# Optimization experiments

Hardware: AMD Instinct MI355X
Metric: run time of the kernel (lower is better)

Reference implementation:

```python
import jax, jax.numpy as jnp
import numpy as np

# dimensions (match init_kwargs / input_specs)
K = 25        # number of observation events
N_PER = 2048  # observations per event
B = 4096      # batch (sample_idx length)
D = 64        # input_dim
NDIM = 8      # memory_dim
H = D * NDIM  # hidden = 512
STEPS = 2     # euler ODE steps between consecutive obs_times
DT = 0.01
LOG_SQRT_2PI = 0.9189385332046727  # log(sqrt(2*pi))


def _xavier(key, shape):
    lim = np.sqrt(6.0 / (shape[0] + shape[1])).astype(np.float32)
    return jax.random.uniform(key, shape, jnp.float32, -lim, lim)


def setup_inputs() -> dict:
    key = jax.random.key(0)
    ks = jax.random.split(key, 10)
    # unique per-event indices (matches torch scatter-assign semantics)
    rng = np.random.RandomState(0)
    batch_idx = jnp.asarray(
        np.stack([rng.permutation(B)[:N_PER] for _ in range(K)]).reshape(-1),
        jnp.int32)
    return {
        "obs_times": jnp.arange(1, K + 1, dtype=jnp.float32) * (STEPS * DT),
        "event_pt": jnp.arange(K + 1, dtype=jnp.int32) * N_PER,
        "sample_idx": jnp.arange(B, dtype=jnp.int32),
        "X": jax.random.normal(ks[0], (K * N_PER, D), jnp.float32),
        "M": (jax.random.uniform(ks[1], (K * N_PER, D)) < 0.8).astype(jnp.float32),
        "batch_idx": batch_idx,
        # ODEFunc: Linear(H,H) -> Tanh -> Linear(H,H)
        "W_ode1": _xavier(ks[2], (H, H)), "b_ode1": jnp.zeros((H,), jnp.float32),
        "W_ode2": _xavier(ks[3], (H, H)), "b_ode2": jnp.zeros((H,), jnp.float32),
        # GRUCell(D, H)
        "W_ih": _xavier(ks[4], (3 * H, D)), "W_hh": _xavier(ks[5], (3 * H, H)),
        "b_ih": jnp.zeros((3 * H,), jnp.float32), "b_hh": jnp.zeros((3 * H,), jnp.float32),
        # p_model: Linear(H,H) -> ReLU -> (dropout=0) -> Linear(H, 2D)
        "Wp1": _xavier(ks[6], (H, H)), "bp1": jnp.zeros((H,), jnp.float32),
        "Wp2": _xavier(ks[7], (2 * D, H)), "bp2": jnp.zeros((2 * D,), jnp.float32),
    }


def reference(obs_times, event_pt, sample_idx, X, M, batch_idx,
              W_ode1, b_ode1, W_ode2, b_ode2,
              W_ih, W_hh, b_ih, b_hh, Wp1, bp1, Wp2, bp2):
    Xr = X.reshape(K, N_PER, D)
    Mr = M.reshape(K, N_PER, D)
    idx = batch_idx.reshape(K, N_PER)

    def ode_func(h):  # Linear -> Tanh -> Linear
        return jnp.tanh(h @ W_ode1.T + b_ode1) @ W_ode2.T + b_ode2

    def gru(x, h):  # torch GRUCell
        gi = x @ W_ih.T + b_ih
        gh = h @ W_hh.T + b_hh
        i_r, i_z, i_n = jnp.split(gi, 3, axis=1)
        h_r, h_z, h_n = jnp.split(gh, 3, axis=1)
        r = jax.nn.sigmoid(i_r + h_r)
        z = jax.nn.sigmoid(i_z + h_z)
        n = jnp.tanh(i_n + r * h_n)
        return (1.0 - z) * n + z * h

    def event_step(carry, inp):
        h, loss, m_tot = carry
        X_obs, M_obs, i_obs = inp
        # euler odeint over [0, dt], STEPS times to reach obs_time
        for _ in range(STEPS):
            h = h + DT * ode_func(h)
        # likelihood head on all samples, gather observed ones
        p = jax.nn.relu(h @ Wp1.T + bp1) @ Wp2.T + bp2       # [B, 2D]
        p_obs = p[i_obs]                                      # [N_PER, 2D]
        mean, logvar = jnp.split(p_obs, 2, axis=1)
        sigma = jnp.exp(0.5 * logvar)
        error = (X_obs - mean) / sigma
        losses = 0.5 * ((error * error + logvar + 2.0 * LOG_SQRT_2PI) * M_obs)
        # GRU update only on observed indices (scatter)
        h = h.at[i_obs].set(gru(X_obs, h[i_obs]))
        return (h, loss + losses.sum(), m_tot + M_obs.sum()), None

    h0 = jnp.zeros((B, H), jnp.float32)
    (h, loss, m_tot), _ = jax.lax.scan(event_step, (h0, jnp.float32(0.0), jnp.float32(0.0)), (Xr, Mr, idx))
    return (loss / m_tot, jnp.float32(0.0))
```

## Files before the change

kernel.cpp:

```cpp
#include <hip/hip_runtime.h>
#include <cstdint>
#include <cstddef>

#define BATCH 4096
#define DIM 64
#define HID 512
#define NPER 2048
#define KEV 25
#define DT_C 0.01f
#define LOG_SQRT_2PI_C 0.9189385332046727f

typedef __attribute__((ext_vector_type(8))) short short8;
typedef __attribute__((ext_vector_type(4))) float f32x4;

#define MFMA(a, b, c) __builtin_amdgcn_mfma_f32_16x16x32_bf16(a, b, c, 0, 0, 0)
#define BARRIER() __builtin_amdgcn_s_barrier()
#define SCHED0()  __builtin_amdgcn_sched_barrier(0)

__device__ __forceinline__ ushort f2bf(float f) {
    uint32_t u = __float_as_uint(f);
    u += 0x7FFF + ((u >> 16) & 1);
    return (ushort)(u >> 16);
}
__device__ __forceinline__ float sigmoidf_(float x) { return 1.0f / (1.0f + expf(-x)); }

__device__ __forceinline__ void gload_lds16(const ushort* g, ushort* l) {
    __builtin_amdgcn_global_load_lds(
        (const __attribute__((address_space(1))) void*)g,
        (__attribute__((address_space(3))) void*)l, 16, 0, 0);
}
__device__ __forceinline__ void wait_vm(int n) {
    if (n == 8)      asm volatile("s_waitcnt vmcnt(8)" ::: "memory");
    else if (n == 7) asm volatile("s_waitcnt vmcnt(7)" ::: "memory");
    else if (n == 6) asm volatile("s_waitcnt vmcnt(6)" ::: "memory");
    else if (n == 4) asm volatile("s_waitcnt vmcnt(4)" ::: "memory");
    else             asm volatile("s_waitcnt vmcnt(0)" ::: "memory");
}

__device__ __forceinline__ short8 frag64(const ushort* lds, int row, int ks, int lane) {
    int slot = ((ks << 2) + (lane >> 4)) ^ (row & 7);
    return *(const short8*)&lds[row * 64 + slot * 8];
}
__device__ __forceinline__ short8 frag128(const ushort* lds, int row, int ks, int lane) {
    int slot = ((ks << 2) + (lane >> 4)) ^ (row & 7);
    return *(const short8*)&lds[row * 128 + slot * 8];
}

__device__ __forceinline__ void stage128(
    const ushort* g, int row0, int k0, int w, int lane, ushort* lds)
{
    #pragma unroll
    for (int gg = 0; gg < 4; ++gg) {
        int row = row0 + w * 16 + gg * 4 + (lane >> 4);
        int slot = (lane & 15) ^ (row & 7);
        gload_lds16(g + (size_t)row * HID + k0 + slot * 8,
                    &lds[(w * 16 + gg * 4) * 128]);
    }
}

__device__ __forceinline__ void gemm_bk128(
    ushort* A0, ushort* A1, ushort* B0, ushort* B1,
    int w, int lane, int wr, int wc,
    const ushort* Ag, int arow0, const ushort* Bg, int brow0,
    f32x4 acc[2][2])
{
    stage128(Ag, arow0, 0, w, lane, A0);
    stage128(Bg, brow0, 0, w, lane, B0);
    stage128(Ag, arow0, 128, w, lane, A1);
    stage128(Bg, brow0, 128, w, lane, B1);
    for (int t = 0; t < 4; ++t) {
        wait_vm((t < 3) ? 8 : 0);
        BARRIER();
        SCHED0();
        const ushort* Ab = (t & 1) ? A1 : A0;
        const ushort* Bb = (t & 1) ? B1 : B0;
        short8 af[2][4], bf[2][4];
        #pragma unroll
        for (int mi = 0; mi < 2; ++mi) {
            int r = wr * 32 + mi * 16 + (lane & 15);
            #pragma unroll
            for (int ks = 0; ks < 4; ++ks) af[mi][ks] = frag128(Ab, r, ks, lane);
        }
        #pragma unroll
        for (int ni = 0; ni < 2; ++ni) {
            int c = wc * 32 + ni * 16 + (lane & 15);
            #pragma unroll
            for (int ks = 0; ks < 4; ++ks) bf[ni][ks] = frag128(Bb, c, ks, lane);
        }
        #pragma unroll
        for (int ks = 0; ks < 4; ++ks)
            #pragma unroll
            for (int mi = 0; mi < 2; ++mi)
                #pragma unroll
                for (int ni = 0; ni < 2; ++ni)
                    acc[mi][ni] = MFMA(af[mi][ks], bf[ni][ks], acc[mi][ni]);
        SCHED0();
        BARRIER();
        if (t + 2 < 4) {
            stage128(Ag, arow0, (t + 2) * 128, w, lane, (t & 1) ? A1 : A0);
            stage128(Bg, brow0, (t + 2) * 128, w, lane, (t & 1) ? B1 : B0);
        }
    }
}

__global__ __launch_bounds__(256) void fuse1(
    const ushort* __restrict__ hb, const ushort* __restrict__ W1,
    const float* __restrict__ b1, ushort* __restrict__ tbb,
    const ushort* __restrict__ hgb, const ushort* __restrict__ Wp1,
    const float* __restrict__ bp1, ushort* __restrict__ qb, int mode)
{
    __shared__ __align__(16) ushort smem[32768];
    ushort* A0 = smem;         ushort* A1 = smem + 8192;
    ushort* B0 = smem + 16384; ushort* B1 = smem + 24576;
    const int tid = threadIdx.x, lane = tid & 63, w = tid >> 6;
    const int wr = w >> 1, wc = w & 1;
    const int bid = blockIdx.x;

    bool isQ; int b;
    if (mode == 2)      { isQ = true;  b = bid; }
    else if (bid < 512) { isQ = false; b = bid; }
    else                { isQ = true;  b = bid - 512; }
    const ushort* A = isQ ? hgb : hb;
    const ushort* W = isQ ? Wp1 : W1;
    const float* bias = isQ ? bp1 : b1;
    const int r0 = (b >> 3) * 64, c0 = (b & 7) * 64;

    f32x4 acc[2][2] = {};
    gemm_bk128(A0, A1, B0, B1, w, lane, wr, wc, A, r0, W, c0, acc);

    #pragma unroll
    for (int mi = 0; mi < 2; ++mi)
        #pragma unroll
        for (int ni = 0; ni < 2; ++ni) {
            const int c = c0 + wc * 32 + ni * 16 + (lane & 15);
            const float bv = bias[c];
            #pragma unroll
            for (int ii = 0; ii < 4; ++ii) {
                const int r = r0 + wr * 32 + mi * 16 + ((lane >> 4) << 2) + ii;
                const size_t o = (size_t)r * HID + c;
                float v = acc[mi][ni][ii] + bv;
                if (!isQ) tbb[o] = f2bf(tanhf(v));
                else      qb[o]  = f2bf(fmaxf(v, 0.0f));
            }
        }
}

__global__ __launch_bounds__(256) void fuse2(
    const ushort* __restrict__ tbb, const ushort* __restrict__ W2,
    const float* __restrict__ b2, float* __restrict__ h, ushort* __restrict__ hb,
    const int* __restrict__ inv, ushort* __restrict__ hgb,
    const ushort* __restrict__ qb, const ushort* __restrict__ Wp2,
    const float* __restrict__ bp2, const float* __restrict__ Xp,
    const float* __restrict__ Mp, float* __restrict__ sums, int mode)
{
    __shared__ __align__(16) ushort smem[32768];
    const int tid = threadIdx.x, lane = tid & 63, w = tid >> 6;
    const int wr = w >> 1, wc = w & 1;
    const int bid = blockIdx.x;

    bool isP; int b;
    if (mode == 2)      { isP = true;  b = bid; }
    else if (bid < 512) { isP = false; b = bid; }
    else                { isP = true;  b = bid - 512; }

    if (!isP) {
        ushort* A0 = smem;         ushort* A1 = smem + 8192;
        ushort* B0 = smem + 16384; ushort* B1 = smem + 24576;
        const int r0 = (b >> 3) * 64, c0 = (b & 7) * 64;
        f32x4 acc[2][2] = {};
        gemm_bk128(A0, A1, B0, B1, w, lane, wr, wc, tbb, r0, W2, c0, acc);
        #pragma unroll
        for (int mi = 0; mi < 2; ++mi)
            #pragma unroll
            for (int ni = 0; ni < 2; ++ni) {
                const int c = c0 + wc * 32 + ni * 16 + (lane & 15);
                const float bv = b2[c];
                #pragma unroll
                for (int ii = 0; ii < 4; ++ii) {
                    const int r = r0 + wr * 32 + mi * 16 + ((lane >> 4) << 2) + ii;
                    const size_t o = (size_t)r * HID + c;
                    float nh = h[o] + DT_C * (acc[mi][ni][ii] + bv);
                    h[o] = nh;
                    ushort bv16 = f2bf(nh);
                    hb[o] = bv16;
                    if (inv) {
                        int iv = inv[r];
                        if (iv >= 0) hgb[(size_t)iv * HID + c] = bv16;
                    }
                }
            }
        return;
    }

    ushort* A0 = smem;        ushort* A1 = smem + 4096;
    ushort* B0 = smem + 8192; ushort* B1 = smem + 16384;
    const int srow = lane >> 3, sg = ((lane & 7) ^ srow) << 3;
    const int r0t = b * 64;
    const int arow = w * 16 + srow;

    auto stage = [&](int bb, int k0) {
        ushort* A = bb ? A1 : A0; ushort* B = bb ? B1 : B0;
        gload_lds16(qb + (size_t)(r0t + arow) * HID + k0 + sg, &A[(w * 16) * 64]);
        gload_lds16(qb + (size_t)(r0t + arow + 8) * HID + k0 + sg, &A[(w * 16 + 8) * 64]);
        #pragma unroll
        for (int j = 0; j < 4; ++j) {
            int g = w * 4 + j;
            int rw = g * 8 + srow;
            gload_lds16(Wp2 + (size_t)rw * HID + k0 + (((lane & 7) ^ (rw & 7)) << 3),
                        &B[g * 8 * 64]);
        }
    };
    f32x4 acc[2][4] = {};
    stage(0, 0);
    stage(1, 64);
    for (int t = 0; t < 8; ++t) {
        wait_vm((t < 7) ? 6 : 0);
        BARRIER();
        SCHED0();
        const ushort* Ab = (t & 1) ? A1 : A0;
        const ushort* Bb = (t & 1) ? B1 : B0;
        short8 af[2][2], bf[4][2];
        #pragma unroll
        for (int mi = 0; mi < 2; ++mi) {
            int r = wr * 32 + mi * 16 + (lane & 15);
            af[mi][0] = frag64(Ab, r, 0, lane);
            af[mi][1] = frag64(Ab, r, 1, lane);
        }
        #pragma unroll
        for (int ni = 0; ni < 4; ++ni) {
            int c = wc * 64 + ni * 16 + (lane & 15);
            bf[ni][0] = frag64(Bb, c, 0, lane);
            bf[ni][1] = frag64(Bb, c, 1, lane);
        }
        #pragma unroll
        for (int ks = 0; ks < 2; ++ks)
            #pragma unroll
            for (int mi = 0; mi < 2; ++mi)
                #pragma unroll
                for (int ni = 0; ni < 4; ++ni)
                    acc[mi][ni] = MFMA(af[mi][ks], bf[ni][ks], acc[mi][ni]);
        SCHED0();
        BARRIER();
        if (t + 2 < 8) stage(t & 1, (t + 2) * 64);
    }

    float* Plds = (float*)smem;
    #pragma unroll
    for (int mi = 0; mi < 2; ++mi)
        #pragma unroll
        for (int ni = 0; ni < 4; ++ni) {
            int c = wc * 64 + ni * 16 + (lane & 15);
            float bv = bp2[c];
            #pragma unroll
            for (int ii = 0; ii < 4; ++ii) {
                int r = wr * 32 + mi * 16 + ((lane >> 4) << 2) + ii;
                Plds[r * 128 + c] = acc[mi][ni][ii] + bv;
            }
        }
    __syncthreads();

    float local = 0.0f;
    for (int t = tid; t < 64 * 64; t += 256) {
        int r = t >> 6, jj = t & 63;
        float mean = Plds[r * 128 + jj];
        float lv   = Plds[r * 128 + 64 + jj];
        int g = r0t + r;
        float err = (Xp[(size_t)g * 64 + jj] - mean) * expf(-0.5f * lv);
        local += 0.5f * (err * err + lv + 2.0f * LOG_SQRT_2PI_C) * Mp[(size_t)g * 64 + jj];
    }
    #pragma unroll
    for (int o = 32; o > 0; o >>= 1) local += __shfl_down(local, o);
    if (lane == 0) atomicAdd(sums, local);
}

__global__ __launch_bounds__(256) void gru_all(
    const ushort* __restrict__ hgb, const ushort* __restrict__ Xbk,
    const int* __restrict__ idx,
    const ushort* __restrict__ Whh, const ushort* __restrict__ Wih,
    const float* __restrict__ bih, const float* __restrict__ bhh,
    float* __restrict__ h, ushort* __restrict__ hb)
{
    __shared__ __align__(16) ushort smem[28672];
    const int tid = threadIdx.x, lane = tid & 63, w = tid >> 6;
    const int srow = lane >> 3, sg = ((lane & 7) ^ srow) << 3;
    const int bid = blockIdx.x;
    const int r0t = (bid >> 3) * 32, c0 = (bid & 7) * 64;

    auto stage = [&](int b, int p) {
        ushort* A = smem + b * 2048;
        ushort* B = smem + 4096 + b * 12288;
        if (p < 8) {
            gload_lds16(hgb + (size_t)(r0t + w * 8 + srow) * HID + p * 64 + sg,
                        &A[(w * 8) * 64]);
            #pragma unroll
            for (int j = 0; j < 6; ++j) {
                int glid = w * 6 + j;
                int g = glid >> 3, rg = (glid & 7) * 8 + srow;
                gload_lds16(Whh + (size_t)(g * 512 + c0 + rg) * HID + p * 64 + sg,
                            &B[glid * 8 * 64]);
            }
        } else {
            gload_lds16(Xbk + (size_t)(r0t + w * 8 + srow) * DIM + sg, &A[(w * 8) * 64]);
            #pragma unroll
            for (int j = 0; j < 6; ++j) {
                int glid = w * 6 + j;
                int g = glid >> 3, rg = (glid & 7) * 8 + srow;
                gload_lds16(Wih + (size_t)(g * 512 + c0 + rg) * DIM + sg,
                            &B[glid * 8 * 64]);
            }
        }
    };

    f32x4 aR[2] = {}, aZ[2] = {}, aNh[2] = {}, aNx[2] = {};
    stage(0, 0);
    stage(1, 1);
    for (int t = 0; t < 8; ++t) {
        wait_vm((t < 7) ? 7 : 7);
        BARRIER();
        SCHED0();
        const ushort* Ab = smem + (t & 1) * 2048;
        short8 af[2][2];
        #pragma unroll
        for (int mi = 0; mi < 2; ++mi) {
            int r = mi * 16 + (lane & 15);
            af[mi][0] = frag64(Ab, r, 0, lane);
            af[mi][1] = frag64(Ab, r, 1, lane);
        }
        const int c_l = w * 16 + (lane & 15);
        #pragma unroll
        for (int g = 0; g < 3; ++g) {
            const ushort* Bb = smem + 4096 + (t & 1) * 12288 + g * 4096;
            short8 bf0 = frag64(Bb, c_l, 0, lane);
            short8 bf1 = frag64(Bb, c_l, 1, lane);
            #pragma unroll
            for (int mi = 0; mi < 2; ++mi) {
                f32x4& a = (g == 0) ? aR[mi] : (g == 1) ? aZ[mi] : aNh[mi];
                a = MFMA(af[mi][0], bf0, a);
                a = MFMA(af[mi][1], bf1, a);
            }
        }
        SCHED0();
        BARRIER();
        if (t + 2 <= 8) stage(t & 1, t + 2);
    }
    {
        wait_vm(0);
        BARRIER();
        SCHED0();
        const ushort* Ab = smem;
        short8 af[2][2];
        #pragma unroll
        for (int mi = 0; mi < 2; ++mi) {
            int r = mi * 16 + (lane & 15);
            af[mi][0] = frag64(Ab, r, 0, lane);
            af[mi][1] = frag64(Ab, r, 1, lane);
        }
        const int c_l = w * 16 + (lane & 15);
        #pragma unroll
        for (int g = 0; g < 3; ++g) {
            const ushort* Bb = smem + 4096 + g * 4096;
            short8 bf0 = frag64(Bb, c_l, 0, lane);
            short8 bf1 = frag64(Bb, c_l, 1, lane);
            #pragma unroll
            for (int mi = 0; mi < 2; ++mi) {
                f32x4& a = (g == 0) ? aR[mi] : (g == 1) ? aZ[mi] : aNx[mi];
                a = MFMA(af[mi][0], bf0, a);
                a = MFMA(af[mi][1], bf1, a);
            }
        }
    }

    {
        const int c = c0 + w * 16 + (lane & 15);
        const float bR = bih[c] + bhh[c];
        const float bZ = bih[512 + c] + bhh[512 + c];
        const float bNx = bih[1024 + c], bNh = bhh[1024 + c];
        #pragma unroll
        for (int mi = 0; mi < 2; ++mi)
            #pragma unroll
            for (int ii = 0; ii < 4; ++ii) {
                const int iobs = r0t + mi * 16 + ((lane >> 4) << 2) + ii;
                const int gr = idx[iobs];
                float r = sigmoidf_(aR[mi][ii] + bR);
                float z = sigmoidf_(aZ[mi][ii] + bZ);
                float n = tanhf(aNx[mi][ii] + bNx + r * (aNh[mi][ii] + bNh));
                const size_t o = (size_t)gr * HID + c;
                float nh = (1.0f - z) * n + z * h[o];
                h[o] = nh;
                hb[o] = f2bf(nh);
            }
    }
}

__device__ __forceinline__ void block_atomic_sum(float v, float* acc) {
    __shared__ float red[4];
    #pragma unroll
    for (int off = 32; off > 0; off >>= 1) v += __shfl_down(v, off);
    int lane = threadIdx.x & 63, wid = threadIdx.x >> 6;
    if (lane == 0) red[wid] = v;
    __syncthreads();
    if (threadIdx.x == 0) atomicAdd(acc, red[0] + red[1] + red[2] + red[3]);
}

__global__ __launch_bounds__(256) void f2b4_kernel(
    const float* __restrict__ s, ushort* __restrict__ d, int n4)
{
    int t = blockIdx.x * 256 + threadIdx.x;
    if (t >= n4) return;
    float4 v = ((const float4*)s)[t];
    ushort4 o; o.x = f2bf(v.x); o.y = f2bf(v.y); o.z = f2bf(v.z); o.w = f2bf(v.w);
    ((ushort4*)d)[t] = o;
}

__global__ __launch_bounds__(256) void msum_kernel(
    const float* __restrict__ M, int n, float* __restrict__ m_acc)
{
    float v = 0.0f;
    for (int t = blockIdx.x * 256 + threadIdx.x; t < n; t += gridDim.x * 256)
        v += M[t];
    block_atomic_sum(v, m_acc);
}

__global__ __launch_bounds__(256) void inv_scatter(
    const int* __restrict__ bidx, int* __restrict__ inv)
{
    int t = blockIdx.x * 256 + threadIdx.x;
    if (t >= KEV * NPER) return;
    int e = t >> 11, i = t & (NPER - 1);
    inv[(size_t)e * BATCH + bidx[t]] = i;
}

__global__ void finalize_kernel(const float* __restrict__ sums, float* __restrict__ out) {
    if (threadIdx.x == 0) { out[0] = sums[0] / sums[1]; out[1] = 0.0f; }
}

extern "C" void kernel_launch(void* const* d_in, const int* in_sizes, int n_in,
                              void* d_out, int out_size, void* d_ws, size_t ws_size,
                              hipStream_t stream) {
    const float* X      = (const float*)d_in[3];
    const float* M      = (const float*)d_in[4];
    const int* batch_idx= (const int*)  d_in[5];
    const float* W_ode1 = (const float*)d_in[6];
    const float* b_ode1 = (const float*)d_in[7];
    const float* W_ode2 = (const float*)d_in[8];
    const float* b_ode2 = (const float*)d_in[9];
    const float* W_ih   = (const float*)d_in[10];
    const float* W_hh   = (const float*)d_in[11];
    const float* b_ih   = (const float*)d_in[12];
    const float* b_hh   = (const float*)d_in[13];
    const float* Wp1    = (const float*)d_in[14];
    const float* bp1    = (const float*)d_in[15];
    const float* Wp2    = (const float*)d_in[16];
    const float* bp2    = (const float*)d_in[17];
    float* out = (float*)d_out;

    float* ws    = (float*)d_ws;
    float* h     = ws;
    float* sums  = h + (size_t)BATCH * HID;
    int*   inv   = (int*)(sums + 16);
    ushort* hb   = (ushort*)(inv + (size_t)KEV * BATCH);
    ushort* tbb  = hb  + (size_t)BATCH * HID;
    ushort* qb   = tbb + (size_t)BATCH * HID;
    ushort* hgb  = qb  + (size_t)NPER * HID;
    ushort* Xb   = hgb + (size_t)NPER * HID;
    ushort* W1b  = Xb  + (size_t)KEV * NPER * DIM;
    ushort* W2b  = W1b + (size_t)HID * HID;
    ushort* Wp1b = W2b + (size_t)HID * HID;
    ushort* Wp2b = Wp1b + (size_t)HID * HID;
    ushort* Wihb = Wp2b + (size_t)2 * DIM * HID;
    ushort* Whhb = Wihb + (size_t)3 * HID * DIM;

    hipMemsetAsync(h,    0, (size_t)BATCH * HID * sizeof(float), stream);
    hipMemsetAsync(hb,   0, (size_t)BATCH * HID * sizeof(ushort), stream);
    hipMemsetAsync(sums, 0, 2 * sizeof(float), stream);
    hipMemsetAsync(inv,  0xFF, (size_t)KEV * BATCH * sizeof(int), stream);

    dim3 blk(256);
    auto cvt = [&](const float* s, ushort* d, size_t n) {
        f2b4_kernel<<<dim3((unsigned)((n / 4 + 255) / 256)), blk, 0, stream>>>(s, d, (int)(n / 4));
    };
    cvt(W_ode1, W1b,  (size_t)HID * HID);
    cvt(W_ode2, W2b,  (size_t)HID * HID);
    cvt(Wp1,    Wp1b, (size_t)HID * HID);
    cvt(Wp2,    Wp2b, (size_t)2 * DIM * HID);
    cvt(W_ih,   Wihb, (size_t)3 * HID * DIM);
    cvt(W_hh,   Whhb, (size_t)3 * HID * HID);
    cvt(X,      Xb,   (size_t)KEV * NPER * DIM);

    msum_kernel<<<1024, blk, 0, stream>>>(M, KEV * NPER * DIM, sums + 1);
    inv_scatter<<<(KEV * NPER + 255) / 256, blk, 0, stream>>>(batch_idx, inv);

    for (int k = 0; k < KEV; ++k) {
        const ushort* Xbk = Xb + (size_t)k * NPER * DIM;
        const int*   idxk = batch_idx + (size_t)k * NPER;
        int* invk = inv + (size_t)k * BATCH;
        const float* Xp = X + (size_t)(k > 0 ? k - 1 : 0) * NPER * DIM;
        const float* Mp = M + (size_t)(k > 0 ? k - 1 : 0) * NPER * DIM;
        const int m1 = (k > 0) ? 1 : 0;

        fuse1<<<dim3(m1 ? 768 : 512), blk, 0, stream>>>(
            hb, W1b, b_ode1, tbb, hgb, Wp1b, bp1, qb, m1);
        fuse2<<<dim3(m1 ? 544 : 512), blk, 0, stream>>>(
            tbb, W2b, b_ode2, h, hb, nullptr, hgb,
            qb, Wp2b, bp2, Xp, Mp, sums, m1);
        fuse1<<<dim3(512), blk, 0, stream>>>(
            hb, W1b, b_ode1, tbb, hgb, Wp1b, bp1, qb, 0);
        fuse2<<<dim3(512), blk, 0, stream>>>(
            tbb, W2b, b_ode2, h, hb, invk, hgb,
            qb, Wp2b, bp2, Xp, Mp, sums, 0);
        gru_all<<<dim3(512), blk, 0, stream>>>(
            hgb, Xbk, idxk, Whhb, Wihb, b_ih, b_hh, h, hb);
    }

    {
        const float* Xp = X + (size_t)(KEV - 1) * NPER * DIM;
        const float* Mp = M + (size_t)(KEV - 1) * NPER * DIM;
        fuse1<<<dim3(256), blk, 0, stream>>>(
            hb, W1b, b_ode1, tbb, hgb, Wp1b, bp1, qb, 2);
        fuse2<<<dim3(32), blk, 0, stream>>>(
            tbb, W2b, b_ode2, h, hb, nullptr, hgb,
            qb, Wp2b, bp2, Xp, Mp, sums, 2);
    }

    finalize_kernel<<<1, 64, 0, stream>>>(sums, out);
}
```

Baseline: 1.943 ms.

## Restructure GRU kernel: load weights directly to registers, halve row tile

The GRU kernel no longer stages the Whh/Wih weight tiles through LDS. Each lane now reads its B fragments straight from global memory into registers and double-buffers them in registers. Only the small activation tile goes through LDS. The row tile shrinks from 32 to 16, doubling the grid to 1024 blocks, which cuts LDS footprint and raises parallelism but reduces weight reuse per block. Global weight loads are uncoalesced per-lane 16-byte reads and rely on caching, and traffic to the weights doubles.

```diff
diff --git a/kernel.cpp b/kernel.cpp
--- a/kernel.cpp
+++ b/kernel.cpp
@@ -31,7 +31,6 @@
 }
 __device__ __forceinline__ void wait_vm(int n) {
     if (n == 8)      asm volatile("s_waitcnt vmcnt(8)" ::: "memory");
-    else if (n == 7) asm volatile("s_waitcnt vmcnt(7)" ::: "memory");
     else if (n == 6) asm volatile("s_waitcnt vmcnt(6)" ::: "memory");
     else if (n == 4) asm volatile("s_waitcnt vmcnt(4)" ::: "memory");
     else             asm volatile("s_waitcnt vmcnt(0)" ::: "memory");
@@ -44,6 +43,10 @@
 __device__ __forceinline__ short8 frag128(const ushort* lds, int row, int ks, int lane) {
     int slot = ((ks << 2) + (lane >> 4)) ^ (row & 7);
     return *(const short8*)&lds[row * 128 + slot * 8];
+}
+__device__ __forceinline__ short8 bglob(const ushort* B, int col, int ldb, int k0, int ks, int lane) {
+    int slot = (ks << 2) + (lane >> 4);
+    return *(const short8*)&B[(size_t)col * ldb + k0 + slot * 8];
 }
 
 __device__ __forceinline__ void stage128(
@@ -280,115 +283,75 @@
     const float* __restrict__ bih, const float* __restrict__ bhh,
     float* __restrict__ h, ushort* __restrict__ hb)
 {
-    __shared__ __align__(16) ushort smem[28672];
+    __shared__ __align__(16) ushort Asm[2][16 * 64];
     const int tid = threadIdx.x, lane = tid & 63, w = tid >> 6;
     const int srow = lane >> 3, sg = ((lane & 7) ^ srow) << 3;
     const int bid = blockIdx.x;
-    const int r0t = (bid >> 3) * 32, c0 = (bid & 7) * 64;
-
-    auto stage = [&](int b, int p) {
-        ushort* A = smem + b * 2048;
-        ushort* B = smem + 4096 + b * 12288;
-        if (p < 8) {
-            gload_lds16(hgb + (size_t)(r0t + w * 8 + srow) * HID + p * 64 + sg,
-                        &A[(w * 8) * 64]);
-            #pragma unroll
-            for (int j = 0; j < 6; ++j) {
-                int glid = w * 6 + j;
-                int g = glid >> 3, rg = (glid & 7) * 8 + srow;
-                gload_lds16(Whh + (size_t)(g * 512 + c0 + rg) * HID + p * 64 + sg,
-                            &B[glid * 8 * 64]);
+    const int r0t = (bid >> 3) * 16, c0 = (bid & 7) * 64;
+    const int cB = c0 + w * 16 + (lane & 15);
+
+    auto stageA = [&](int b, int p) {
+        if (w < 2) {
+            const ushort* src = (p < 8)
+                ? hgb + (size_t)(r0t + w * 8 + srow) * HID + p * 64 + sg
+                : Xbk + (size_t)(r0t + w * 8 + srow) * DIM + sg;
+            gload_lds16(src, &Asm[b][(w * 8) * 64]);
+        }
+    };
+    short8 bcur[3][2], bnxt[3][2];
+    auto loadB = [&](short8 d[3][2], int p) {
+        #pragma unroll
+        for (int g = 0; g < 3; ++g)
+            #pragma unroll
+            for (int ks = 0; ks < 2; ++ks)
+                d[g][ks] = (p < 8)
+                    ? bglob(Whh, g * 512 + cB, HID, p * 64, ks, lane)
+                    : bglob(Wih, g * 512 + cB, DIM, 0, ks, lane);
+    };
+
+    f32x4 aR = {}, aZ = {}, aNh = {}, aNx = {};
+    stageA(0, 0);
+    loadB(bcur, 0);
+    stageA(1, 1);
+    __syncthreads();
+
+    #pragma unroll
+    for (int t = 0; t < 9; ++t) {
+        if (t < 8) loadB(bnxt, t + 1);
+        const ushort* Ab = &Asm[t & 1][0];
+        short8 af0 = frag64(Ab, lane & 15, 0, lane);
+        short8 af1 = frag64(Ab, lane & 15, 1, lane);
+        aR = MFMA(af0, bcur[0][0], aR); aR = MFMA(af1, bcur[0][1], aR);
+        aZ = MFMA(af0, bcur[1][0], aZ); aZ = MFMA(af1, bcur[1][1], aZ);
+        if (t < 8) { aNh = MFMA(af0, bcur[2][0], aNh); aNh = MFMA(af1, bcur[2][1], aNh); }
+        else       { aNx = MFMA(af0, bcur[2][0], aNx); aNx = MFMA(af1, bcur[2][1], aNx); }
+        if (t < 8) {
+            #pragma unroll
+            for (int g = 0; g < 3; ++g) {
+                bcur[g][0] = bnxt[g][0];
+                bcur[g][1] = bnxt[g][1];
             }
-        } else {
-            gload_lds16(Xbk + (size_t)(r0t + w * 8 + srow) * DIM + sg, &A[(w * 8) * 64]);
-            #pragma unroll
-            for (int j = 0; j < 6; ++j) {
-                int glid = w * 6 + j;
-                int g = glid >> 3, rg = (glid & 7) * 8 + srow;
-                gload_lds16(Wih + (size_t)(g * 512 + c0 + rg) * DIM + sg,
-                            &B[glid * 8 * 64]);
-            }
-        }
-    };
-
-    f32x4 aR[2] = {}, aZ[2] = {}, aNh[2] = {}, aNx[2] = {};
-    stage(0, 0);
-    stage(1, 1);
-    for (int t = 0; t < 8; ++t) {
-        wait_vm((t < 7) ? 7 : 7);
-        BARRIER();
-        SCHED0();
-        const ushort* Ab = smem + (t & 1) * 2048;
-        short8 af[2][2];
-        #pragma unroll
-        for (int mi = 0; mi < 2; ++mi) {
-            int r = mi * 16 + (lane & 15);
-            af[mi][0] = frag64(Ab, r, 0, lane);
-            af[mi][1] = frag64(Ab, r, 1, lane);
-        }
-        const int c_l = w * 16 + (lane & 15);
-        #pragma unroll
-        for (int g = 0; g < 3; ++g) {
-            const ushort* Bb = smem + 4096 + (t & 1) * 12288 + g * 4096;
-            short8 bf0 = frag64(Bb, c_l, 0, lane);
-            short8 bf1 = frag64(Bb, c_l, 1, lane);
-            #pragma unroll
-            for (int mi = 0; mi < 2; ++mi) {
-                f32x4& a = (g == 0) ? aR[mi] : (g == 1) ? aZ[mi] : aNh[mi];
-                a = MFMA(af[mi][0], bf0, a);
-                a = MFMA(af[mi][1], bf1, a);
-            }
-        }
-        SCHED0();
-        BARRIER();
-        if (t + 2 <= 8) stage(t & 1, t + 2);
-    }
+            __syncthreads();
+            stageA(t & 1, t + 2);
+        }
+    }
+
     {
-        wait_vm(0);
-        BARRIER();
-        SCHED0();
-        const ushort* Ab = smem;
-        short8 af[2][2];
-        #pragma unroll
-        for (int mi = 0; mi < 2; ++mi) {
-            int r = mi * 16 + (lane & 15);
-            af[mi][0] = frag64(Ab, r, 0, lane);
-            af[mi][1] = frag64(Ab, r, 1, lane);
-        }
-        const int c_l = w * 16 + (lane & 15);
-        #pragma unroll
-        for (int g = 0; g < 3; ++g) {
-            const ushort* Bb = smem + 4096 + g * 4096;
-            short8 bf0 = frag64(Bb, c_l, 0, lane);
-            short8 bf1 = frag64(Bb, c_l, 1, lane);
-            #pragma unroll
-            for (int mi = 0; mi < 2; ++mi) {
-                f32x4& a = (g == 0) ? aR[mi] : (g == 1) ? aZ[mi] : aNx[mi];
-                a = MFMA(af[mi][0], bf0, a);
-                a = MFMA(af[mi][1], bf1, a);
-            }
-        }
-    }
-
-    {
-        const int c = c0 + w * 16 + (lane & 15);
-        const float bR = bih[c] + bhh[c];
-        const float bZ = bih[512 + c] + bhh[512 + c];
-        const float bNx = bih[1024 + c], bNh = bhh[1024 + c];
-        #pragma unroll
-        for (int mi = 0; mi < 2; ++mi)
-            #pragma unroll
-            for (int ii = 0; ii < 4; ++ii) {
-                const int iobs = r0t + mi * 16 + ((lane >> 4) << 2) + ii;
-                const int gr = idx[iobs];
-                float r = sigmoidf_(aR[mi][ii] + bR);
-                float z = sigmoidf_(aZ[mi][ii] + bZ);
-                float n = tanhf(aNx[mi][ii] + bNx + r * (aNh[mi][ii] + bNh));
-                const size_t o = (size_t)gr * HID + c;
-                float nh = (1.0f - z) * n + z * h[o];
-                h[o] = nh;
-                hb[o] = f2bf(nh);
-            }
+        const float bR = bih[cB] + bhh[cB];
+        const float bZ = bih[512 + cB] + bhh[512 + cB];
+        const float bNx = bih[1024 + cB], bNh = bhh[1024 + cB];
+        #pragma unroll
+        for (int ii = 0; ii < 4; ++ii) {
+            const int iobs = r0t + ((lane >> 4) << 2) + ii;
+            const int gr = idx[iobs];
+            float r = sigmoidf_(aR[ii] + bR);
+            float z = sigmoidf_(aZ[ii] + bZ);
+            float n = tanhf(aNx[ii] + bNx + r * (aNh[ii] + bNh));
+            const size_t o = (size_t)gr * HID + cB;
+            float nh = (1.0f - z) * n + z * h[o];
+            h[o] = nh;
+            hb[o] = f2bf(nh);
+        }
     }
 }
 
@@ -508,7 +471,7 @@
         fuse2<<<dim3(512), blk, 0, stream>>>(
             tbb, W2b, b_ode2, h, hb, invk, hgb,
             qb, Wp2b, bp2, Xp, Mp, sums, 0);
-        gru_all<<<dim3(512), blk, 0, stream>>>(
+        gru_all<<<dim3(1024), blk, 0, stream>>>(
             hgb, Xbk, idxk, Whhb, Wihb, b_ih, b_hh, h, hb);
     }
 
```

Result: slower. 2.293 ms (+18.0%).
